# Kernel tuning notes

Hardware: AMD Instinct MI355X
Metric: run time of the kernel (lower is better)

The kernel has to match this reference:

```python
import jax, jax.numpy as jnp
import numpy as np

# ---- static config (mirrors init_kwargs) ----
N, E, G = 10000, 120000, 32
F_NODE, F_EDGE = 64, 16
H, HEADS, L, R = 128, 4, 3, 4
ID_DIM, REL_DIM = 32, 8
NUM_IDS, NUM_CLASSES = 5000, 10
FFN_H, HEAD_H = 256, 128
GRID_SIZE, SPLINE_ORDER = 5, 3
NC = GRID_SIZE + SPLINE_ORDER  # n spline coeffs per input = 8
GRID = jnp.asarray(np.arange(-SPLINE_ORDER, GRID_SIZE + SPLINE_ORDER + 1, dtype=np.float32) * (2.0 / GRID_SIZE) - 1.0)  # [12], grid_range=(-1,1)
NEG = -1e30


def _b_splines(x, grid):
    # x: [B, in] -> bases [B, in, NC]  (Cox-de Boor, as in efficient-kan)
    x = x[..., None]
    bases = ((x >= grid[:-1]) & (x < grid[1:])).astype(x.dtype)
    for p in range(1, SPLINE_ORDER + 1):
        left = (x - grid[:-(p + 1)]) / (grid[p:-1] - grid[:-(p + 1)]) * bases[..., :-1]
        right = (grid[p + 1:] - x) / (grid[p + 1:] - grid[1:-p]) * bases[..., 1:]
        bases = left + right
    return bases


def _kan_linear(x, base_w, spline_w, scaler, grid):
    # base path: SiLU(x) @ W_base^T ; spline path: b_splines(x) contracted with scaled spline weights
    base = jax.nn.silu(x) @ base_w.T
    spline = jnp.einsum('big,oig->bo', _b_splines(x, grid), spline_w * scaler[..., None])
    return base + spline


def _ln(x, g, b, eps=1e-5):
    mu = x.mean(-1, keepdims=True)
    var = ((x - mu) ** 2).mean(-1, keepdims=True)
    return (x - mu) * jax.lax.rsqrt(var + eps) * g + b


def _forward(x, edge_attr, id_emb, in_W, in_b, Wl, bl, Wr, br, We, att, gat_bias,
             rel_gate, rel_emb, ln1_g, ln1_b, ln2_g, ln2_b,
             ffn1_base, ffn1_spline, ffn1_scaler, ffn2_base, ffn2_spline, ffn2_scaler,
             ro_g, ro_b, head1_base, head1_spline, head1_scaler, head2_base, head2_spline, head2_scaler,
             id_token, edge_index, edge_type, batch):
    grid = GRID
    # input proj: concat(id embedding) -> Linear -> SiLU (dropout = identity, eval)
    h = jnp.concatenate([x, id_emb[id_token]], axis=-1)
    h = jax.nn.silu(h @ in_W + in_b)
    src, tgt = edge_index[0], edge_index[1]
    for l in range(L):
        gates = jax.nn.softmax(rel_gate[l])  # all relations present
        h_msg = jnp.zeros_like(h)
        for r in range(R):
            # GATv2Conv (heads=4, concat=False, add_self_loops=False)
            xl = (h @ Wl[l, r] + bl[l, r]).reshape(N, HEADS, H)
            xr = (h @ Wr[l, r] + br[l, r]).reshape(N, HEADS, H)
            # edge feature = concat(edge_attr, rel_emb[r]) @ We, split to avoid materializing the concat
            e = (edge_attr @ We[l, r, :F_EDGE] + rel_emb[l, r] @ We[l, r, F_EDGE:]).reshape(E, HEADS, H)
            z = jax.nn.leaky_relu(xl[src] + xr[tgt] + e, 0.2)   # [E, heads, H]
            score = jnp.einsum('ehd,hd->eh', z, att[l, r])
            mask = (edge_type == r)[:, None]
            score = jnp.where(mask, score, NEG)
            m = jax.ops.segment_max(score, tgt, num_segments=N)  # per-target softmax max
            ex = jnp.where(mask, jnp.exp(score - m[tgt]), 0.0)
            denom = jax.ops.segment_sum(ex, tgt, num_segments=N)
            alpha = ex / jnp.maximum(denom[tgt], 1e-16)          # [E, heads]
            agg = jax.ops.segment_sum(xl[src] * alpha[..., None], tgt, num_segments=N)
            h_r = agg.mean(axis=1) + gat_bias[l, r]              # concat=False -> head mean + bias
            h_msg = h_msg + gates[r] * h_r
        h = _ln(h + h_msg, ln1_g[l], ln1_b[l])
        # KAN FFN: KANLinear(H->FFN_H) -> KANLinear(FFN_H->H)
        h_ffn = _kan_linear(h, ffn1_base[l], ffn1_spline[l], ffn1_scaler[l], grid)
        h_ffn = _kan_linear(h_ffn, ffn2_base[l], ffn2_spline[l], ffn2_scaler[l], grid)
        h = _ln(h + h_ffn, ln2_g[l], ln2_b[l])
    # readout: mean+max pool per graph
    cnt = jax.ops.segment_sum(jnp.ones((N,), h.dtype), batch, num_segments=G)
    h_mean = jax.ops.segment_sum(h, batch, num_segments=G) / jnp.maximum(cnt, 1.0)[:, None]
    h_max = jax.ops.segment_max(h, batch, num_segments=G)
    h_max = jnp.where(jnp.isfinite(h_max), h_max, 0.0)
    g = _ln(jnp.concatenate([h_mean, h_max], axis=-1), ro_g, ro_b)
    # KAN head: KANLinear(2H->HEAD_H) -> KANLinear(HEAD_H->NUM_CLASSES)
    g = _kan_linear(g, head1_base, head1_spline, head1_scaler, grid)
    logits = _kan_linear(g, head2_base, head2_spline, head2_scaler, grid)
    return logits


def setup_inputs():
    key = jax.random.key(0)
    ks = iter(jax.random.split(key, 48))
    n = lambda shape, s=0.05: jax.random.normal(next(ks), shape, dtype=jnp.float32) * s
    d = {}
    d['x'] = jax.random.normal(next(ks), (N, F_NODE), dtype=jnp.float32)
    d['edge_attr'] = jax.random.normal(next(ks), (E, F_EDGE), dtype=jnp.float32)
    d['id_token'] = jax.random.randint(next(ks), (N,), 0, NUM_IDS + 1)
    d['edge_index'] = jax.random.randint(next(ks), (2, E), 0, N)
    d['edge_type'] = jax.random.randint(next(ks), (E,), 0, R)
    d['batch'] = jnp.sort(jax.random.randint(next(ks), (N,), 0, G))
    d['id_emb'] = n((NUM_IDS + 1, ID_DIM), 0.1)
    d['in_W'] = n((F_NODE + ID_DIM, H))
    d['in_b'] = jnp.zeros((H,), jnp.float32)
    d['Wl'] = n((L, R, H, HEADS * H)); d['bl'] = jnp.zeros((L, R, HEADS * H), jnp.float32)
    d['Wr'] = n((L, R, H, HEADS * H)); d['br'] = jnp.zeros((L, R, HEADS * H), jnp.float32)
    d['We'] = n((L, R, F_EDGE + REL_DIM, HEADS * H))
    d['att'] = n((L, R, HEADS, H), 0.1)
    d['gat_bias'] = jnp.zeros((L, R, H), jnp.float32)
    d['rel_gate'] = n((L, R), 0.1)
    d['rel_emb'] = n((L, R, REL_DIM), 0.1)
    d['ln1_g'] = jnp.ones((L, H), jnp.float32); d['ln1_b'] = jnp.zeros((L, H), jnp.float32)
    d['ln2_g'] = jnp.ones((L, H), jnp.float32); d['ln2_b'] = jnp.zeros((L, H), jnp.float32)
    d['ffn1_base'] = n((L, FFN_H, H)); d['ffn1_spline'] = n((L, FFN_H, H, NC)); d['ffn1_scaler'] = jnp.ones((L, FFN_H, H), jnp.float32)
    d['ffn2_base'] = n((L, H, FFN_H)); d['ffn2_spline'] = n((L, H, FFN_H, NC)); d['ffn2_scaler'] = jnp.ones((L, H, FFN_H), jnp.float32)
    d['ro_g'] = jnp.ones((2 * H,), jnp.float32); d['ro_b'] = jnp.zeros((2 * H,), jnp.float32)
    d['head1_base'] = n((HEAD_H, 2 * H)); d['head1_spline'] = n((HEAD_H, 2 * H, NC)); d['head1_scaler'] = jnp.ones((HEAD_H, 2 * H), jnp.float32)
    d['head2_base'] = n((NUM_CLASSES, HEAD_H)); d['head2_spline'] = n((NUM_CLASSES, HEAD_H, NC)); d['head2_scaler'] = jnp.ones((NUM_CLASSES, HEAD_H), jnp.float32)
    return d


def reference(x, edge_attr, id_emb, in_W, in_b, Wl, bl, Wr, br, We, att, gat_bias,
              rel_gate, rel_emb, ln1_g, ln1_b, ln2_g, ln2_b,
              ffn1_base, ffn1_spline, ffn1_scaler, ffn2_base, ffn2_spline, ffn2_scaler,
              ro_g, ro_b, head1_base, head1_spline, head1_scaler, head2_base, head2_spline, head2_scaler,
              id_token, edge_index, edge_type, batch):
    return _forward(x, edge_attr, id_emb, in_W, in_b, Wl, bl, Wr, br, We, att, gat_bias,
                    rel_gate, rel_emb, ln1_g, ln1_b, ln2_g, ln2_b,
                    ffn1_base, ffn1_spline, ffn1_scaler, ffn2_base, ffn2_spline, ffn2_scaler,
                    ro_g, ro_b, head1_base, head1_spline, head1_scaler, head2_base, head2_spline, head2_scaler,
                    id_token, edge_index, edge_type, batch)
```

## Files before the change

### kernel.cpp

```cpp
#include <hip/hip_runtime.h>
#include <cstdint>
#include <cstddef>

#define NN      10000
#define NE      120000
#define NG      32
#define FNODE   64
#define FEDGE   16
#define HID     128
#define NHEADS  4
#define NL      3
#define NR      4
#define IDDIM   32
#define RELDIM  8
#define FFNH    256
#define HEADH   128
#define NCLS    10

#define NCHUNK  128
#define SCTOT   (NN * NR)
#define SCBLK   ((SCTOT + 255) / 256)

typedef __attribute__((ext_vector_type(8))) short short8;
typedef __attribute__((ext_vector_type(4))) float floatx4;

__device__ __forceinline__ float silu_f(float x) { return x / (1.f + expf(-x)); }
__device__ __forceinline__ ushort f2bf(float f) {
  unsigned u = __float_as_uint(f);
  return (ushort)((u + 0x7FFFu + ((u >> 16) & 1u)) >> 16);
}
__device__ __forceinline__ float bf2f(ushort h) { return __uint_as_float((unsigned)h << 16); }

__device__ __forceinline__ void kan_bases(float x, float* out8) {
  float bb[11];
#pragma unroll
  for (int j = 0; j < 11; ++j) {
    float t0 = (j - 3) * 0.4f - 1.f;
    float t1 = (j - 2) * 0.4f - 1.f;
    bb[j] = (x >= t0 && x < t1) ? 1.f : 0.f;
  }
  {
    const float inv = 1.f / 0.4f;
#pragma unroll
    for (int j = 0; j < 10; ++j) {
      float tj = (j - 3) * 0.4f - 1.f, tjp1 = (j - 1) * 0.4f - 1.f;
      bb[j] = ((x - tj) * bb[j] + (tjp1 - x) * bb[j + 1]) * inv;
    }
  }
  {
    const float inv = 1.f / 0.8f;
#pragma unroll
    for (int j = 0; j < 9; ++j) {
      float tj = (j - 3) * 0.4f - 1.f, tjp1 = (j) * 0.4f - 1.f;
      bb[j] = ((x - tj) * bb[j] + (tjp1 - x) * bb[j + 1]) * inv;
    }
  }
  {
    const float inv = 1.f / 1.2000001f;
#pragma unroll
    for (int j = 0; j < 8; ++j) {
      float tj = (j - 3) * 0.4f - 1.f, tjp1 = (j + 1) * 0.4f - 1.f;
      bb[j] = ((x - tj) * bb[j] + (tjp1 - x) * bb[j + 1]) * inv;
    }
  }
#pragma unroll
  for (int j = 0; j < 8; ++j) out8[j] = bb[j];
}

__global__ __launch_bounds__(256) void gemm_bf3(
    const ushort* __restrict__ Ahg, const ushort* __restrict__ Alg,
    const ushort* __restrict__ Bhg, const ushort* __restrict__ Blg,
    const float* __restrict__ bias, float* __restrict__ C,
    int M, int K, int N) {
  constexpr int LDA = 68;
  __shared__ __align__(16) ushort Ah[128 * LDA];
  __shared__ __align__(16) ushort Al[128 * LDA];
  __shared__ __align__(16) ushort Bh[64 * LDA];
  __shared__ __align__(16) ushort Bl[64 * LDA];
  const int tid = threadIdx.x;
  const int lane = tid & 63, wave = tid >> 6;
  const int lrow = lane & 15, quad = lane >> 4;
  const int bm = blockIdx.y * 128, bn = blockIdx.x * 64;
  floatx4 acc[2][4] = {};
  for (int k0 = 0; k0 < K; k0 += 64) {
#pragma unroll
    for (int i = 0; i < 4; ++i) {
      int c = tid + i * 256;
      int row = c >> 3, col8 = c & 7;
      int gr = bm + row;
      uint4 vh = make_uint4(0, 0, 0, 0), vl = make_uint4(0, 0, 0, 0);
      if (gr < M) {
        vh = *(const uint4*)(Ahg + (size_t)gr * K + k0 + col8 * 8);
        vl = *(const uint4*)(Alg + (size_t)gr * K + k0 + col8 * 8);
      }
      *(uint4*)&Ah[row * LDA + col8 * 8] = vh;
      *(uint4*)&Al[row * LDA + col8 * 8] = vl;
    }
#pragma unroll
    for (int i = 0; i < 2; ++i) {
      int c = tid + i * 256;
      int row = c >> 3, col8 = c & 7;
      *(uint4*)&Bh[row * LDA + col8 * 8] = *(const uint4*)(Bhg + (size_t)(bn + row) * K + k0 + col8 * 8);
      *(uint4*)&Bl[row * LDA + col8 * 8] = *(const uint4*)(Blg + (size_t)(bn + row) * K + k0 + col8 * 8);
    }
    __syncthreads();
#pragma unroll
    for (int kk = 0; kk < 64; kk += 32) {
      int kof = kk + quad * 8;
      const int ra0 = (wave * 32 + lrow) * LDA + kof;
      const int ra1 = (wave * 32 + 16 + lrow) * LDA + kof;
      short8 ah0 = *(const short8*)&Ah[ra0];
      short8 ah1 = *(const short8*)&Ah[ra1];
      short8 al0 = *(const short8*)&Al[ra0];
      short8 al1 = *(const short8*)&Al[ra1];
      short8 bh[4], blo[4];
#pragma unroll
      for (int nt = 0; nt < 4; ++nt) {
        int rb = (nt * 16 + lrow) * LDA + kof;
        bh[nt]  = *(const short8*)&Bh[rb];
        blo[nt] = *(const short8*)&Bl[rb];
      }
#pragma unroll
      for (int nt = 0; nt < 4; ++nt) {
        acc[0][nt] = __builtin_amdgcn_mfma_f32_16x16x32_bf16(ah0, bh[nt],  acc[0][nt], 0, 0, 0);
        acc[1][nt] = __builtin_amdgcn_mfma_f32_16x16x32_bf16(ah1, bh[nt],  acc[1][nt], 0, 0, 0);
        acc[0][nt] = __builtin_amdgcn_mfma_f32_16x16x32_bf16(al0, bh[nt],  acc[0][nt], 0, 0, 0);
        acc[1][nt] = __builtin_amdgcn_mfma_f32_16x16x32_bf16(al1, bh[nt],  acc[1][nt], 0, 0, 0);
        acc[0][nt] = __builtin_amdgcn_mfma_f32_16x16x32_bf16(ah0, blo[nt], acc[0][nt], 0, 0, 0);
        acc[1][nt] = __builtin_amdgcn_mfma_f32_16x16x32_bf16(ah1, blo[nt], acc[1][nt], 0, 0, 0);
      }
    }
    __syncthreads();
  }
#pragma unroll
  for (int mt = 0; mt < 2; ++mt) {
#pragma unroll
    for (int nt = 0; nt < 4; ++nt) {
#pragma unroll
      for (int reg = 0; reg < 4; ++reg) {
        int row = bm + wave * 32 + mt * 16 + quad * 4 + reg;
        int col = bn + nt * 16 + lrow;
        if (row < M) {
          float v = acc[mt][nt][reg];
          if (bias) v += bias[col];
          C[(size_t)row * N + col] = v;
        }
      }
    }
  }
}

template<int BM, int SPLIT>
__global__ __launch_bounds__(256) void gemm_kan(
    const float* __restrict__ A, const ushort* __restrict__ Bhg, const ushort* __restrict__ Blg,
    float* __restrict__ C, int M, int In, int N) {
  const int K = In * 9;
  const int ntiles = K >> 6;
  const int per = (ntiles + SPLIT - 1) / SPLIT;
  const int kt0 = blockIdx.z * per;
  const int kt1 = (kt0 + per < ntiles) ? (kt0 + per) : ntiles;
  constexpr int LDA = 68;
  __shared__ __align__(16) ushort Ah[BM * LDA];
  __shared__ __align__(16) ushort Al[BM * LDA];
  __shared__ __align__(16) ushort Bh[64 * LDA];
  __shared__ __align__(16) ushort Bl[64 * LDA];
  const int tid = threadIdx.x;
  const int lane = tid & 63, wave = tid >> 6;
  const int lrow = lane & 15, quad = lane >> 4;
  const int bm = blockIdx.y * BM, bn = blockIdx.x * 64;
  constexpr int MT = BM / 64;
  floatx4 acc[MT][4] = {};
  for (int kt = kt0; kt < kt1; ++kt) {
    int k0 = kt << 6;
    if (k0 < In) {
#pragma unroll
      for (int i = 0; i < BM / 16; ++i) {
        int c = tid + i * 256;
        int row = c >> 4, col4 = c & 15;
        int gr = bm + row;
        float4 v = make_float4(0.f, 0.f, 0.f, 0.f);
        if (gr < M) v = *(const float4*)(A + (size_t)gr * In + k0 + col4 * 4);
        float vv[4] = {silu_f(v.x), silu_f(v.y), silu_f(v.z), silu_f(v.w)};
        ushort h0 = f2bf(vv[0]), h1 = f2bf(vv[1]), h2 = f2bf(vv[2]), h3 = f2bf(vv[3]);
        ushort l0 = f2bf(vv[0] - bf2f(h0)), l1 = f2bf(vv[1] - bf2f(h1));
        ushort l2 = f2bf(vv[2] - bf2f(h2)), l3 = f2bf(vv[3] - bf2f(h3));
        *(uint2*)&Ah[row * LDA + col4 * 4] =
          make_uint2((unsigned)h0 | ((unsigned)h1 << 16), (unsigned)h2 | ((unsigned)h3 << 16));
        *(uint2*)&Al[row * LDA + col4 * 4] =
          make_uint2((unsigned)l0 | ((unsigned)l1 << 16), (unsigned)l2 | ((unsigned)l3 << 16));
      }
    } else {
      int i0 = (k0 - In) >> 3;
      if (tid < BM * 2) {
        int row = tid >> 1, half = tid & 1;
        int gr = bm + row;
        float4 v = make_float4(0.f, 0.f, 0.f, 0.f);
        if (gr < M) v = *(const float4*)(A + (size_t)gr * In + i0 + half * 4);
        float vv[4] = {v.x, v.y, v.z, v.w};
#pragma unroll
        for (int jj = 0; jj < 4; ++jj) {
          float b8[8];
          kan_bases(vv[jj], b8);
          unsigned hu[4], lu[4];
#pragma unroll
          for (int q = 0; q < 4; ++q) {
            ushort ha = f2bf(b8[2 * q]), hb = f2bf(b8[2 * q + 1]);
            ushort la = f2bf(b8[2 * q] - bf2f(ha)), lb = f2bf(b8[2 * q + 1] - bf2f(hb));
            hu[q] = (unsigned)ha | ((unsigned)hb << 16);
            lu[q] = (unsigned)la | ((unsigned)lb << 16);
          }
          int cbase = (half * 4 + jj) * 8;
          *(uint4*)&Ah[row * LDA + cbase] = make_uint4(hu[0], hu[1], hu[2], hu[3]);
          *(uint4*)&Al[row * LDA + cbase] = make_uint4(lu[0], lu[1], lu[2], lu[3]);
        }
      }
    }
#pragma unroll
    for (int i = 0; i < 2; ++i) {
      int c = tid + i * 256;
      int row = c >> 3, col8 = c & 7;
      *(uint4*)&Bh[row * LDA + col8 * 8] = *(const uint4*)(Bhg + (size_t)(bn + row) * K + k0 + col8 * 8);
      *(uint4*)&Bl[row * LDA + col8 * 8] = *(const uint4*)(Blg + (size_t)(bn + row) * K + k0 + col8 * 8);
    }
    __syncthreads();
#pragma unroll
    for (int kk = 0; kk < 64; kk += 32) {
      int kof = kk + quad * 8;
      short8 ah[MT], al[MT];
#pragma unroll
      for (int mt = 0; mt < MT; ++mt) {
        int ra = (wave * (BM / 4) + mt * 16 + lrow) * LDA + kof;
        ah[mt] = *(const short8*)&Ah[ra];
        al[mt] = *(const short8*)&Al[ra];
      }
      short8 bh[4], blo[4];
#pragma unroll
      for (int nt = 0; nt < 4; ++nt) {
        int rb = (nt * 16 + lrow) * LDA + kof;
        bh[nt]  = *(const short8*)&Bh[rb];
        blo[nt] = *(const short8*)&Bl[rb];
      }
#pragma unroll
      for (int nt = 0; nt < 4; ++nt) {
#pragma unroll
        for (int mt = 0; mt < MT; ++mt) {
          acc[mt][nt] = __builtin_amdgcn_mfma_f32_16x16x32_bf16(ah[mt], bh[nt],  acc[mt][nt], 0, 0, 0);
          acc[mt][nt] = __builtin_amdgcn_mfma_f32_16x16x32_bf16(al[mt], bh[nt],  acc[mt][nt], 0, 0, 0);
          acc[mt][nt] = __builtin_amdgcn_mfma_f32_16x16x32_bf16(ah[mt], blo[nt], acc[mt][nt], 0, 0, 0);
        }
      }
    }
    __syncthreads();
  }
#pragma unroll
  for (int mt = 0; mt < MT; ++mt) {
#pragma unroll
    for (int nt = 0; nt < 4; ++nt) {
#pragma unroll
      for (int reg = 0; reg < 4; ++reg) {
        int row = bm + wave * (BM / 4) + mt * 16 + quad * 4 + reg;
        int col = bn + nt * 16 + lrow;
        if (row < M) atomicAdd(&C[(size_t)row * N + col], acc[mt][nt][reg]);
      }
    }
  }
}

__global__ void conv_wT2(const float* __restrict__ Wl, const float* __restrict__ Wr,
                         const float* __restrict__ bl, const float* __restrict__ br,
                         ushort* __restrict__ WTh, ushort* __restrict__ WTl,
                         float* __restrict__ bout, int total) {
  int i = blockIdx.x * 256 + threadIdx.x;
  if (i >= total) return;
  int g2 = i / (2048 * 128), rem = i % (2048 * 128);
  int n = rem >> 7, k = rem & 127;
  int l = g2 >> 1, pair = g2 & 1;
  int r = pair * 2 + (n >> 10);
  int nsub = n & 1023;
  int nn = nsub & 511;
  int g = l * NR + r;
  const float* W = (nsub < 512) ? Wl : Wr;
  float v = W[(size_t)g * 65536 + (size_t)k * 512 + nn];
  ushort hi = f2bf(v);
  WTh[i] = hi;
  WTl[i] = f2bf(v - bf2f(hi));
  if (k == 0) bout[g2 * 2048 + n] = ((nsub < 512) ? bl : br)[g * 512 + nn];
}

__global__ void build_kan_wT(const float* __restrict__ base_w, const float* __restrict__ spline_w,
                             const float* __restrict__ scaler,
                             ushort* __restrict__ BTh, ushort* __restrict__ BTl,
                             int In, int Out) {
  int i = blockIdx.x * 256 + threadIdx.x;
  if (i >= In * 9 * Out) return;
  int o = i / (In * 9), k = i % (In * 9);
  float v;
  if (k < In) v = base_w[(size_t)o * In + k];
  else {
    int q = k - In, ii = q >> 3, gq = q & 7;
    v = spline_w[((size_t)o * In + ii) * 8 + gq] * scaler[(size_t)o * In + ii];
  }
  ushort hi = f2bf(v);
  BTh[i] = hi;
  BTl[i] = f2bf(v - bf2f(hi));
}

__global__ __launch_bounds__(128) void input_proj(
    const float* __restrict__ x, const float* __restrict__ id_emb,
    const int* __restrict__ id_token, const float* __restrict__ inW,
    const float* __restrict__ inb, float* __restrict__ h,
    ushort* __restrict__ hh, ushort* __restrict__ hl) {
  int n = blockIdx.x, j = threadIdx.x;
  __shared__ float s[FNODE + IDDIM];
  if (j < FNODE) s[j] = x[(size_t)n * FNODE + j];
  else if (j < FNODE + IDDIM) s[j] = id_emb[(size_t)id_token[n] * IDDIM + (j - FNODE)];
  __syncthreads();
  float acc = inb[j];
#pragma unroll
  for (int k = 0; k < FNODE + IDDIM; ++k) acc = fmaf(s[k], inW[k * HID + j], acc);
  float v = silu_f(acc);
  h[(size_t)n * HID + j] = v;
  ushort hi = f2bf(v);
  hh[(size_t)n * HID + j] = hi;
  hl[(size_t)n * HID + j] = f2bf(v - bf2f(hi));
}

__global__ __launch_bounds__(512) void layer_prep(
    const float* __restrict__ rel_gate, const float* __restrict__ gat_bias,
    const float* __restrict__ rel_emb, const float* __restrict__ We, int l,
    float* __restrict__ gates, float* __restrict__ msg_bias, float* __restrict__ erel) {
  int j = threadIdx.x;
  float g[NR]; float mx = -1e30f;
  for (int r = 0; r < NR; ++r) { g[r] = rel_gate[l * NR + r]; mx = fmaxf(mx, g[r]); }
  float s = 0.f;
  for (int r = 0; r < NR; ++r) { g[r] = expf(g[r] - mx); s += g[r]; }
  for (int r = 0; r < NR; ++r) g[r] /= s;
  if (j < NR) gates[j] = g[j];
  if (j < HID) {
    float b = 0.f;
    for (int r = 0; r < NR; ++r) b = fmaf(g[r], gat_bias[((size_t)(l * NR + r)) * HID + j], b);
    msg_bias[j] = b;
  }
  for (int r = 0; r < NR; ++r) {
    const float* Wer = We + ((size_t)(l * NR + r)) * 24 * 512;
    const float* re  = rel_emb + (l * NR + r) * RELDIM;
    float acc = 0.f;
#pragma unroll
    for (int q = 0; q < RELDIM; ++q) acc = fmaf(re[q], Wer[(FEDGE + q) * 512 + j], acc);
    erel[r * 512 + j] = acc;
  }
}

__global__ void fill_zero(float* __restrict__ p, int n) {
  int i = blockIdx.x * 256 + threadIdx.x;
  if (i < n) p[i] = 0.f;
}
__global__ void fill_zero_i(int* __restrict__ p, int n) {
  int i = blockIdx.x * 256 + threadIdx.x;
  if (i < n) p[i] = 0;
}

__global__ void csr_count2(const int* __restrict__ eidx, const int* __restrict__ etype,
                           int* __restrict__ deg2) {
  int e = blockIdx.x * 256 + threadIdx.x;
  if (e < NE) atomicAdd(&deg2[eidx[NE + e] * NR + etype[e]], 1);
}

__global__ __launch_bounds__(256) void scan_p1(const int* __restrict__ deg2,
                                               int* __restrict__ tmp_incl, int* __restrict__ bsum) {
  __shared__ int ps[256];
  int t = threadIdx.x, blk = blockIdx.x;
  int i = blk * 256 + t;
  int v = (i < SCTOT) ? deg2[i] : 0;
  ps[t] = v;
  __syncthreads();
  for (int o = 1; o < 256; o <<= 1) {
    int u = (t >= o) ? ps[t - o] : 0;
    __syncthreads();
    ps[t] += u;
    __syncthreads();
  }
  if (i < SCTOT) tmp_incl[i] = ps[t];
  if (t == 255) bsum[blk] = ps[255];
}
__global__ __launch_bounds__(256) void scan_p2(const int* __restrict__ bsum, int* __restrict__ boff) {
  __shared__ int ps[256];
  int t = threadIdx.x;
  int v = (t < SCBLK) ? bsum[t] : 0;
  ps[t] = v;
  __syncthreads();
  for (int o = 1; o < 256; o <<= 1) {
    int u = (t >= o) ? ps[t - o] : 0;
    __syncthreads();
    ps[t] += u;
    __syncthreads();
  }
  if (t < SCBLK) boff[t] = ps[t] - v;
}
__global__ __launch_bounds__(256) void scan_p3(const int* __restrict__ deg2,
                                               const int* __restrict__ tmp_incl,
                                               const int* __restrict__ boff,
                                               int* __restrict__ in_off2, int* __restrict__ cursor2) {
  int t = threadIdx.x, blk = blockIdx.x;
  int i = blk * 256 + t;
  if (i < SCTOT) {
    int excl = boff[blk] + tmp_incl[i] - deg2[i];
    in_off2[i] = excl;
    cursor2[i] = excl;
  }
  if (i == 0) in_off2[SCTOT] = NE;
}

__global__ void csr_scatter2(const int* __restrict__ eidx, const int* __restrict__ etype,
                             int* __restrict__ cursor2,
                             int* __restrict__ in_e2, int* __restrict__ in_s2) {
  int e = blockIdx.x * 256 + threadIdx.x;
  if (e < NE) {
    int pos = atomicAdd(&cursor2[eidx[NE + e] * NR + etype[e]], 1);
    in_e2[pos] = e;
    in_s2[pos] = eidx[e];
  }
}

__global__ __launch_bounds__(256) void gat_node4(
    const int* __restrict__ in_off2, const int* __restrict__ in_e2, const int* __restrict__ in_s2,
    const float* __restrict__ eattr, const float* __restrict__ xlr,
    const float* __restrict__ We_base, const float* __restrict__ erel_base,
    const float* __restrict__ att_base, const float* __restrict__ gates,
    int rbase, float* __restrict__ hmsg) {
  __shared__ float WeL[16][512];
  __shared__ float attL[512];
  __shared__ float erelL[512];
  int tid = threadIdx.x;
  int rs = blockIdx.y;
  int r = rbase + rs;
  const float* We_r = We_base + (size_t)rs * 24 * 512;
  for (int i = tid; i < 16 * 512; i += 256) WeL[i >> 9][i & 511] = We_r[i];
  for (int i = tid; i < 512; i += 256) {
    attL[i] = att_base[rs * 512 + i];
    erelL[i] = erel_base[rs * 512 + i];
  }
  __syncthreads();
  float gr = gates[r] * 0.25f;
  int lane = tid & 63, wave = tid >> 6;
  int n = blockIdx.x * 4 + wave;
  if (n >= NN) return;
  int roff = rs * 1024;
  float xr[8];
  const float* xrb = xlr + (size_t)n * 2048 + roff + 512;
#pragma unroll
  for (int h = 0; h < 4; ++h) {
    xr[h * 2]     = xrb[h * 128 + lane];
    xr[h * 2 + 1] = xrb[h * 128 + 64 + lane];
  }
  float m[4] = {-1e30f, -1e30f, -1e30f, -1e30f};
  float lsum[4] = {0.f, 0.f, 0.f, 0.f};
  float acc[8] = {0.f, 0.f, 0.f, 0.f, 0.f, 0.f, 0.f, 0.f};
  int e0 = in_off2[n * NR + r], e1 = in_off2[n * NR + r + 1];
  int e_nxt = 0, s_nxt = 0;
  if (e0 < e1) { e_nxt = in_e2[e0]; s_nxt = in_s2[e0]; }
  for (int ii = e0; ii < e1; ++ii) {
    int e = e_nxt, s = s_nxt;
    if (ii + 1 < e1) { e_nxt = in_e2[ii + 1]; s_nxt = in_s2[ii + 1]; }
    const float* xls = xlr + (size_t)s * 2048 + roff;
    float ea[16];
#pragma unroll
    for (int k = 0; k < 16; ++k) ea[k] = eattr[(size_t)e * 16 + k];
    float xlv[8], p[4];
#pragma unroll
    for (int h = 0; h < 4; ++h) {
      float ph = 0.f;
#pragma unroll
      for (int half = 0; half < 2; ++half) {
        int idx = h * 128 + half * 64 + lane;
        float xv = xls[idx];
        xlv[h * 2 + half] = xv;
        float et = erelL[idx];
#pragma unroll
        for (int k = 0; k < 16; ++k) et = fmaf(ea[k], WeL[k][idx], et);
        float z = xv + xr[h * 2 + half] + et;
        z = (z > 0.f) ? z : 0.2f * z;
        ph = fmaf(z, attL[idx], ph);
      }
      p[h] = ph;
    }
#pragma unroll
    for (int h = 0; h < 4; ++h) {
#pragma unroll
      for (int o = 32; o > 0; o >>= 1) p[h] += __shfl_xor(p[h], o, 64);
    }
#pragma unroll
    for (int h = 0; h < 4; ++h) {
      float sh = p[h];
      float mn = fmaxf(m[h], sh);
      float sc = expf(m[h] - mn);
      float we = expf(sh - mn);
      m[h] = mn;
      lsum[h] = lsum[h] * sc + we;
      acc[h * 2]     = acc[h * 2] * sc + we * xlv[h * 2];
      acc[h * 2 + 1] = acc[h * 2 + 1] * sc + we * xlv[h * 2 + 1];
    }
  }
  float o0 = 0.f, o1 = 0.f;
#pragma unroll
  for (int h = 0; h < 4; ++h) {
    float inv = 1.f / fmaxf(lsum[h], 1e-16f);
    o0 += acc[h * 2] * inv;
    o1 += acc[h * 2 + 1] * inv;
  }
  size_t base = (size_t)n * HID;
  atomicAdd(&hmsg[base + lane],      gr * o0);
  atomicAdd(&hmsg[base + 64 + lane], gr * o1);
}

__global__ __launch_bounds__(64) void ln128(
    float* __restrict__ h, const float* __restrict__ add, const float* __restrict__ bvec,
    const float* __restrict__ g, const float* __restrict__ b,
    ushort* __restrict__ hh, ushort* __restrict__ hl) {
  int n = blockIdx.x, lane = threadIdx.x;
  size_t base = (size_t)n * HID;
  float x0 = h[base + lane] + add[base + lane];
  float x1 = h[base + 64 + lane] + add[base + 64 + lane];
  if (bvec) { x0 += bvec[lane]; x1 += bvec[64 + lane]; }
  float s = x0 + x1;
#pragma unroll
  for (int m = 32; m > 0; m >>= 1) s += __shfl_xor(s, m, 64);
  float mu = s * (1.f / 128.f);
  float d0 = x0 - mu, d1 = x1 - mu;
  float q = d0 * d0 + d1 * d1;
#pragma unroll
  for (int m = 32; m > 0; m >>= 1) q += __shfl_xor(q, m, 64);
  float inv = 1.f / sqrtf(q * (1.f / 128.f) + 1e-5f);
  float o0 = d0 * inv * g[lane] + b[lane];
  float o1 = d1 * inv * g[64 + lane] + b[64 + lane];
  h[base + lane]      = o0;
  h[base + 64 + lane] = o1;
  if (hh) {
    ushort i0 = f2bf(o0), i1 = f2bf(o1);
    hh[base + lane] = i0;        hh[base + 64 + lane] = i1;
    hl[base + lane] = f2bf(o0 - bf2f(i0));
    hl[base + 64 + lane] = f2bf(o1 - bf2f(i1));
  }
}

__global__ void expand_f32(const float* __restrict__ v, float* __restrict__ u, int In, int rows) {
  int i = blockIdx.x * 256 + threadIdx.x;
  if (i >= rows * In) return;
  int n = i / In, c = i % In;
  float x = v[(size_t)n * In + c];
  size_t base = (size_t)n * In * 9;
  u[base + c] = silu_f(x);
  float b8[8];
  kan_bases(x, b8);
  float* ub = u + base + In + (size_t)c * 8;
#pragma unroll
  for (int gq = 0; gq < 8; ++gq) ub[gq] = b8[gq];
}

__global__ __launch_bounds__(128) void pool_part(
    const float* __restrict__ h, const int* __restrict__ batch,
    float* __restrict__ psum, float* __restrict__ pmax, float* __restrict__ pcnt) {
  __shared__ float sS[NG][HID];
  __shared__ float sM[NG][HID];
  __shared__ int sC[NG];
  int d = threadIdx.x, blk = blockIdx.x;
  const float NEGINF = __uint_as_float(0xff800000u);
  for (int i = d; i < NG * HID; i += 128) {
    ((float*)sS)[i] = 0.f;
    ((float*)sM)[i] = NEGINF;
  }
  if (d < NG) sC[d] = 0;
  __syncthreads();
  const int CH = (NN + NCHUNK - 1) / NCHUNK;
  int n0 = blk * CH, n1 = (n0 + CH < NN) ? n0 + CH : NN;
  for (int n = n0; n < n1; ++n) {
    int g = batch[n];
    float v = h[(size_t)n * HID + d];
    sS[g][d] += v;
    sM[g][d] = fmaxf(sM[g][d], v);
    if (d == 0) sC[g]++;
  }
  __syncthreads();
  for (int i = d; i < NG * HID; i += 128) {
    psum[(size_t)blk * NG * HID + i] = ((float*)sS)[i];
    pmax[(size_t)blk * NG * HID + i] = ((float*)sM)[i];
  }
  if (d < NG) pcnt[blk * NG + d] = (float)sC[d];
}

__global__ __launch_bounds__(256) void pool_final2(
    const float* __restrict__ psum, const float* __restrict__ pmax,
    const float* __restrict__ pcnt, const float* __restrict__ rog,
    const float* __restrict__ rob, float* __restrict__ gvec) {
  int g = blockIdx.x, j = threadIdx.x;
  __shared__ float rb[256];
  float x;
  if (j < HID) {
    float s = 0.f, cn = 0.f;
    for (int c = 0; c < NCHUNK; ++c) {
      s += psum[(size_t)c * NG * HID + g * HID + j];
      cn += pcnt[c * NG + g];
    }
    x = s / fmaxf(cn, 1.f);
  } else {
    float mx = __uint_as_float(0xff800000u);
    for (int c = 0; c < NCHUNK; ++c)
      mx = fmaxf(mx, pmax[(size_t)c * NG * HID + g * HID + (j - HID)]);
    x = (mx > -1e38f) ? mx : 0.f;
  }
  rb[j] = x; __syncthreads();
  for (int st = 128; st > 0; st >>= 1) { if (j < st) rb[j] += rb[j + st]; __syncthreads(); }
  float mu = rb[0] * (1.f / 256.f); __syncthreads();
  float d = x - mu;
  rb[j] = d * d; __syncthreads();
  for (int st = 128; st > 0; st >>= 1) { if (j < st) rb[j] += rb[j + st]; __syncthreads(); }
  float var = rb[0] * (1.f / 256.f);
  float inv = 1.f / sqrtf(var + 1e-5f);
  gvec[(size_t)g * 256 + j] = d * inv * rog[j] + rob[j];
}

__global__ __launch_bounds__(256) void kan_head_w(
    const float* __restrict__ u, const float* __restrict__ base_w,
    const float* __restrict__ spline_w, const float* __restrict__ scaler,
    float* __restrict__ out, int In, int Out, int npairs) {
  int wid = blockIdx.x * 4 + (threadIdx.x >> 6);
  if (wid >= npairs) return;
  int g = wid / Out, o = wid % Out;
  int lane = threadIdx.x & 63;
  const float* ug = u + (size_t)g * In * 9;
  const float* bw = base_w + (size_t)o * In;
  const float* sp = spline_w + (size_t)o * In * 8;
  const float* sc = scaler + (size_t)o * In;
  float acc = 0.f;
  for (int i = lane; i < In; i += 64) acc = fmaf(ug[i], bw[i], acc);
  const float* us = ug + In;
  for (int k = lane; k < In * 8; k += 64) {
    int i = k >> 3;
    acc = fmaf(us[k], sp[k] * sc[i], acc);
  }
#pragma unroll
  for (int off2 = 32; off2 > 0; off2 >>= 1) acc += __shfl_xor(acc, off2, 64);
  if (lane == 0) out[(size_t)g * Out + o] = acc;
}

extern "C" void kernel_launch(void* const* d_in, const int* in_sizes, int n_in,
                              void* d_out, int out_size, void* d_ws, size_t ws_size,
                              hipStream_t stream) {
  const float* x         = (const float*)d_in[0];
  const float* edge_attr = (const float*)d_in[1];
  const int*   id_token  = (const int*)  d_in[2];
  const int*   edge_index= (const int*)  d_in[3];
  const int*   edge_type = (const int*)  d_in[4];
  const int*   batch     = (const int*)  d_in[5];
  const float* id_emb    = (const float*)d_in[6];
  const float* inW       = (const float*)d_in[7];
  const float* inb       = (const float*)d_in[8];
  const float* Wl        = (const float*)d_in[9];
  const float* bl        = (const float*)d_in[10];
  const float* Wr        = (const float*)d_in[11];
  const float* br        = (const float*)d_in[12];
  const float* We        = (const float*)d_in[13];
  const float* att       = (const float*)d_in[14];
  const float* gat_bias  = (const float*)d_in[15];
  const float* rel_gate  = (const float*)d_in[16];
  const float* rel_emb   = (const float*)d_in[17];
  const float* ln1g      = (const float*)d_in[18];
  const float* ln1b      = (const float*)d_in[19];
  const float* ln2g      = (const float*)d_in[20];
  const float* ln2b      = (const float*)d_in[21];
  const float* ffn1_base = (const float*)d_in[22];
  const float* ffn1_spl  = (const float*)d_in[23];
  const float* ffn1_sc   = (const float*)d_in[24];
  const float* ffn2_base = (const float*)d_in[25];
  const float* ffn2_spl  = (const float*)d_in[26];
  const float* ffn2_sc   = (const float*)d_in[27];
  const float* rog       = (const float*)d_in[28];
  const float* rob       = (const float*)d_in[29];
  const float* h1_base   = (const float*)d_in[30];
  const float* h1_spl    = (const float*)d_in[31];
  const float* h1_sc     = (const float*)d_in[32];
  const float* h2_base   = (const float*)d_in[33];
  const float* h2_spl    = (const float*)d_in[34];
  const float* h2_sc     = (const float*)d_in[35];
  (void)in_sizes; (void)n_in; (void)out_size; (void)ws_size;

  char* wsp = (char*)d_ws;
  size_t off = 0;
  auto carve = [&](size_t bytes) { char* p = wsp + off; off = (off + bytes + 255) & ~(size_t)255; return p; };
  float*    h     = (float*)   carve((size_t)NN * HID * 4);
  ushort*   h_hi  = (ushort*)  carve((size_t)NN * HID * 2);
  ushort*   h_lo  = (ushort*)  carve((size_t)NN * HID * 2);
  float*    hmsg  = (float*)   carve((size_t)NN * HID * 4);
  float*    t1    = (float*)   carve((size_t)NN * FFNH * 4);
  float*    gates = (float*)   carve(NR * 4);
  float*    msgb  = (float*)   carve(HID * 4);
  float*    erel  = (float*)   carve(NR * 512 * 4);
  ushort*   WTh   = (ushort*)  carve((size_t)NL * 2 * 2048 * HID * 2);
  ushort*   WTl   = (ushort*)  carve((size_t)NL * 2 * 2048 * HID * 2);
  float*    blr   = (float*)   carve((size_t)NL * 2 * 2048 * 4);
  ushort*   B1h   = (ushort*)  carve((size_t)FFNH * HID * 9 * 2);
  ushort*   B1l   = (ushort*)  carve((size_t)FFNH * HID * 9 * 2);
  ushort*   B2h   = (ushort*)  carve((size_t)HID * FFNH * 9 * 2);
  ushort*   B2l   = (ushort*)  carve((size_t)HID * FFNH * 9 * 2);
  float*    psum  = (float*)   carve((size_t)NCHUNK * NG * HID * 4);
  float*    pmax  = (float*)   carve((size_t)NCHUNK * NG * HID * 4);
  float*    pcnt  = (float*)   carve((size_t)NCHUNK * NG * 4);
  float*    gvec  = (float*)   carve((size_t)NG * 256 * 4);
  float*    uhead = (float*)   carve((size_t)NG * 256 * 9 * 4);
  float*    thead = (float*)   carve((size_t)NG * HEADH * 4);
  float*    xlr   = (float*)   carve((size_t)NN * 2048 * 4);
  int*      deg2  = (int*)     carve((size_t)SCTOT * 4);
  int*      in_off2=(int*)     carve((size_t)(SCTOT + 1) * 4);
  int*      cursor2=(int*)     carve((size_t)SCTOT * 4);
  int*      tmp_incl=(int*)    carve((size_t)SCTOT * 4);
  int*      bsum  = (int*)     carve((size_t)SCBLK * 4);
  int*      boff  = (int*)     carve((size_t)SCBLK * 4);
  int*      in_e2 = (int*)     carve((size_t)NE * 4);
  int*      in_s2 = (int*)     carve((size_t)NE * 4);

  fill_zero_i<<<(SCTOT + 255) / 256, 256, 0, stream>>>(deg2, SCTOT);
  csr_count2<<<(NE + 255) / 256, 256, 0, stream>>>(edge_index, edge_type, deg2);
  scan_p1<<<SCBLK, 256, 0, stream>>>(deg2, tmp_incl, bsum);
  scan_p2<<<1, 256, 0, stream>>>(bsum, boff);
  scan_p3<<<SCBLK, 256, 0, stream>>>(deg2, tmp_incl, boff, in_off2, cursor2);
  csr_scatter2<<<(NE + 255) / 256, 256, 0, stream>>>(edge_index, edge_type, cursor2, in_e2, in_s2);

  {
    int total = NL * 2 * 2048 * 128;
    conv_wT2<<<(total + 255) / 256, 256, 0, stream>>>(Wl, Wr, bl, br, WTh, WTl, blr, total);
  }

  input_proj<<<NN, 128, 0, stream>>>(x, id_emb, id_token, inW, inb, h, h_hi, h_lo);

  const int MB128 = (NN + 127) / 128;
  const int MB64  = (NN + 63) / 64;
  for (int l = 0; l < NL; ++l) {
    layer_prep<<<1, 512, 0, stream>>>(rel_gate, gat_bias, rel_emb, We, l, gates, msgb, erel);
    fill_zero<<<(NN * HID + 255) / 256, 256, 0, stream>>>(hmsg, NN * HID);
    for (int pair = 0; pair < 2; ++pair) {
      int g2 = l * 2 + pair;
      const ushort* WThp = WTh + (size_t)g2 * 2048 * HID;
      const ushort* WTlp = WTl + (size_t)g2 * 2048 * HID;
      const float* blp   = blr + (size_t)g2 * 2048;
      int rbase = pair * 2;
      gemm_bf3<<<dim3(2048 / 64, MB128), 256, 0, stream>>>(h_hi, h_lo, WThp, WTlp, blp, xlr, NN, HID, 2048);
      gat_node4<<<dim3((NN + 3) / 4, 2), 256, 0, stream>>>(
          in_off2, in_e2, in_s2, edge_attr, xlr,
          We + ((size_t)(l * NR + rbase)) * 24 * 512, erel + rbase * 512,
          att + (size_t)(l * NR + rbase) * 512, gates, rbase, hmsg);
    }
    ln128<<<NN, 64, 0, stream>>>(h, hmsg, msgb, ln1g + l * HID, ln1b + l * HID, nullptr, nullptr);

    build_kan_wT<<<((HID * 9 * FFNH) + 255) / 256, 256, 0, stream>>>(
        ffn1_base + (size_t)l * FFNH * HID, ffn1_spl + (size_t)l * FFNH * HID * 8,
        ffn1_sc + (size_t)l * FFNH * HID, B1h, B1l, HID, FFNH);
    fill_zero<<<(NN * FFNH + 255) / 256, 256, 0, stream>>>(t1, NN * FFNH);
    gemm_kan<128, 3><<<dim3(FFNH / 64, MB128, 3), 256, 0, stream>>>(h, B1h, B1l, t1, NN, HID, FFNH);
    build_kan_wT<<<((FFNH * 9 * HID) + 255) / 256, 256, 0, stream>>>(
        ffn2_base + (size_t)l * HID * FFNH, ffn2_spl + (size_t)l * HID * FFNH * 8,
        ffn2_sc + (size_t)l * HID * FFNH, B2h, B2l, FFNH, HID);
    fill_zero<<<(NN * HID + 255) / 256, 256, 0, stream>>>(hmsg, NN * HID);
    gemm_kan<64, 4><<<dim3(HID / 64, MB64, 4), 256, 0, stream>>>(t1, B2h, B2l, hmsg, NN, FFNH, HID);
    ln128<<<NN, 64, 0, stream>>>(h, hmsg, nullptr, ln2g + l * HID, ln2b + l * HID, h_hi, h_lo);
  }

  pool_part<<<NCHUNK, 128, 0, stream>>>(h, batch, psum, pmax, pcnt);
  pool_final2<<<NG, 256, 0, stream>>>(psum, pmax, pcnt, rog, rob, gvec);
  expand_f32<<<((NG * 256) + 255) / 256, 256, 0, stream>>>(gvec, uhead, 256, NG);
  {
    int npairs = NG * HEADH;
    kan_head_w<<<(npairs + 3) / 4, 256, 0, stream>>>(uhead, h1_base, h1_spl, h1_sc, thead, 256, HEADH, npairs);
  }
  expand_f32<<<((NG * HEADH) + 255) / 256, 256, 0, stream>>>(thead, uhead, HEADH, NG);
  {
    int npairs = NG * NCLS;
    kan_head_w<<<(npairs + 3) / 4, 256, 0, stream>>>(uhead, h2_base, h2_spl, h2_sc, (float*)d_out, HEADH, NCLS, npairs);
  }
}
```

Measured before the change: 1.626 ms.

## Vectorize GAT edge kernel with float4 per-lane channel layout and prefetch

```diff
diff --git a/kernel.cpp b/kernel.cpp
--- a/kernel.cpp
+++ b/kernel.cpp
@@ -422,92 +422,115 @@
   }
 }
 
-__global__ __launch_bounds__(256) void gat_node4(
+__global__ __launch_bounds__(256) void gat_node6(
     const int* __restrict__ in_off2, const int* __restrict__ in_e2, const int* __restrict__ in_s2,
     const float* __restrict__ eattr, const float* __restrict__ xlr,
     const float* __restrict__ We_base, const float* __restrict__ erel_base,
     const float* __restrict__ att_base, const float* __restrict__ gates,
     int rbase, float* __restrict__ hmsg) {
-  __shared__ float WeL[16][512];
-  __shared__ float attL[512];
-  __shared__ float erelL[512];
+  __shared__ __align__(16) float WeL[16 * 512];
+  __shared__ __align__(16) float sAgg[4][512];
   int tid = threadIdx.x;
   int rs = blockIdx.y;
   int r = rbase + rs;
   const float* We_r = We_base + (size_t)rs * 24 * 512;
-  for (int i = tid; i < 16 * 512; i += 256) WeL[i >> 9][i & 511] = We_r[i];
-  for (int i = tid; i < 512; i += 256) {
-    attL[i] = att_base[rs * 512 + i];
-    erelL[i] = erel_base[rs * 512 + i];
-  }
+  for (int i = tid; i < 16 * 512 / 4; i += 256)
+    *(float4*)&WeL[i * 4] = *(const float4*)&We_r[i * 4];
   __syncthreads();
   float gr = gates[r] * 0.25f;
   int lane = tid & 63, wave = tid >> 6;
   int n = blockIdx.x * 4 + wave;
   if (n >= NN) return;
   int roff = rs * 1024;
-  float xr[8];
+  const int cA = lane * 4;
+  const int cB = 256 + lane * 4;
   const float* xrb = xlr + (size_t)n * 2048 + roff + 512;
-#pragma unroll
-  for (int h = 0; h < 4; ++h) {
-    xr[h * 2]     = xrb[h * 128 + lane];
-    xr[h * 2 + 1] = xrb[h * 128 + 64 + lane];
-  }
-  float m[4] = {-1e30f, -1e30f, -1e30f, -1e30f};
-  float lsum[4] = {0.f, 0.f, 0.f, 0.f};
-  float acc[8] = {0.f, 0.f, 0.f, 0.f, 0.f, 0.f, 0.f, 0.f};
-  int e0 = in_off2[n * NR + r], e1 = in_off2[n * NR + r + 1];
-  int e_nxt = 0, s_nxt = 0;
-  if (e0 < e1) { e_nxt = in_e2[e0]; s_nxt = in_s2[e0]; }
-  for (int ii = e0; ii < e1; ++ii) {
-    int e = e_nxt, s = s_nxt;
-    if (ii + 1 < e1) { e_nxt = in_e2[ii + 1]; s_nxt = in_s2[ii + 1]; }
-    const float* xls = xlr + (size_t)s * 2048 + roff;
-    float ea[16];
-#pragma unroll
-    for (int k = 0; k < 16; ++k) ea[k] = eattr[(size_t)e * 16 + k];
-    float xlv[8], p[4];
-#pragma unroll
-    for (int h = 0; h < 4; ++h) {
-      float ph = 0.f;
-#pragma unroll
-      for (int half = 0; half < 2; ++half) {
-        int idx = h * 128 + half * 64 + lane;
-        float xv = xls[idx];
-        xlv[h * 2 + half] = xv;
-        float et = erelL[idx];
-#pragma unroll
-        for (int k = 0; k < 16; ++k) et = fmaf(ea[k], WeL[k][idx], et);
-        float z = xv + xr[h * 2 + half] + et;
-        z = (z > 0.f) ? z : 0.2f * z;
-        ph = fmaf(z, attL[idx], ph);
-      }
-      p[h] = ph;
-    }
-#pragma unroll
-    for (int h = 0; h < 4; ++h) {
-#pragma unroll
-      for (int o = 32; o > 0; o >>= 1) p[h] += __shfl_xor(p[h], o, 64);
-    }
-#pragma unroll
-    for (int h = 0; h < 4; ++h) {
-      float sh = p[h];
-      float mn = fmaxf(m[h], sh);
-      float sc = expf(m[h] - mn);
-      float we = expf(sh - mn);
-      m[h] = mn;
-      lsum[h] = lsum[h] * sc + we;
-      acc[h * 2]     = acc[h * 2] * sc + we * xlv[h * 2];
-      acc[h * 2 + 1] = acc[h * 2 + 1] * sc + we * xlv[h * 2 + 1];
-    }
-  }
-  float o0 = 0.f, o1 = 0.f;
-#pragma unroll
-  for (int h = 0; h < 4; ++h) {
-    float inv = 1.f / fmaxf(lsum[h], 1e-16f);
-    o0 += acc[h * 2] * inv;
-    o1 += acc[h * 2 + 1] * inv;
-  }
+  float4 xrA = *(const float4*)(xrb + cA);
+  float4 xrB = *(const float4*)(xrb + cB);
+  float4 attA = *(const float4*)(att_base + rs * 512 + cA);
+  float4 attB = *(const float4*)(att_base + rs * 512 + cB);
+  float4 erA  = *(const float4*)(erel_base + rs * 512 + cA);
+  float4 erB  = *(const float4*)(erel_base + rs * 512 + cB);
+  float mA = -1e30f, mB = -1e30f, lsA = 0.f, lsB = 0.f;
+  float4 accA = make_float4(0.f, 0.f, 0.f, 0.f);
+  float4 accB = make_float4(0.f, 0.f, 0.f, 0.f);
+  int e0 = in_off2[n * NR + r];
+  int cnt = in_off2[n * NR + r + 1] - e0;
+  float4 pxA, pxB, pe0, pe1, pe2, pe3;
+  int eN = 0, sN = 0;
+  if (cnt > 0) {
+    int eC = in_e2[e0], sC = in_s2[e0];
+    if (cnt > 1) { eN = in_e2[e0 + 1]; sN = in_s2[e0 + 1]; }
+    const float* xls = xlr + (size_t)sC * 2048 + roff;
+    pxA = *(const float4*)(xls + cA);
+    pxB = *(const float4*)(xls + cB);
+    const float4* eap = (const float4*)(eattr + (size_t)eC * 16);
+    pe0 = eap[0]; pe1 = eap[1]; pe2 = eap[2]; pe3 = eap[3];
+  }
+  for (int j = 0; j < cnt; ++j) {
+    float4 xA = pxA, xB = pxB;
+    float ea[16] = {pe0.x, pe0.y, pe0.z, pe0.w, pe1.x, pe1.y, pe1.z, pe1.w,
+                    pe2.x, pe2.y, pe2.z, pe2.w, pe3.x, pe3.y, pe3.z, pe3.w};
+    if (j + 1 < cnt) {
+      int eC = eN, sC = sN;
+      if (j + 2 < cnt) { eN = in_e2[e0 + j + 2]; sN = in_s2[e0 + j + 2]; }
+      const float* xls = xlr + (size_t)sC * 2048 + roff;
+      pxA = *(const float4*)(xls + cA);
+      pxB = *(const float4*)(xls + cB);
+      const float4* eap = (const float4*)(eattr + (size_t)eC * 16);
+      pe0 = eap[0]; pe1 = eap[1]; pe2 = eap[2]; pe3 = eap[3];
+    }
+    float4 etA = erA, etB = erB;
+#pragma unroll
+    for (int k = 0; k < 16; ++k) {
+      float4 wA = *(const float4*)&WeL[k * 512 + cA];
+      float4 wB = *(const float4*)&WeL[k * 512 + cB];
+      etA.x = fmaf(ea[k], wA.x, etA.x); etA.y = fmaf(ea[k], wA.y, etA.y);
+      etA.z = fmaf(ea[k], wA.z, etA.z); etA.w = fmaf(ea[k], wA.w, etA.w);
+      etB.x = fmaf(ea[k], wB.x, etB.x); etB.y = fmaf(ea[k], wB.y, etB.y);
+      etB.z = fmaf(ea[k], wB.z, etB.z); etB.w = fmaf(ea[k], wB.w, etB.w);
+    }
+    float sA, sB;
+    {
+      float z0 = xA.x + xrA.x + etA.x; z0 = (z0 > 0.f) ? z0 : 0.2f * z0;
+      float z1 = xA.y + xrA.y + etA.y; z1 = (z1 > 0.f) ? z1 : 0.2f * z1;
+      float z2 = xA.z + xrA.z + etA.z; z2 = (z2 > 0.f) ? z2 : 0.2f * z2;
+      float z3 = xA.w + xrA.w + etA.w; z3 = (z3 > 0.f) ? z3 : 0.2f * z3;
+      sA = z0 * attA.x + z1 * attA.y + z2 * attA.z + z3 * attA.w;
+      z0 = xB.x + xrB.x + etB.x; z0 = (z0 > 0.f) ? z0 : 0.2f * z0;
+      z1 = xB.y + xrB.y + etB.y; z1 = (z1 > 0.f) ? z1 : 0.2f * z1;
+      z2 = xB.z + xrB.z + etB.z; z2 = (z2 > 0.f) ? z2 : 0.2f * z2;
+      z3 = xB.w + xrB.w + etB.w; z3 = (z3 > 0.f) ? z3 : 0.2f * z3;
+      sB = z0 * attB.x + z1 * attB.y + z2 * attB.z + z3 * attB.w;
+    }
+#pragma unroll
+    for (int o = 1; o <= 16; o <<= 1) {
+      sA += __shfl_xor(sA, o, 64);
+      sB += __shfl_xor(sB, o, 64);
+    }
+    {
+      float mn = fmaxf(mA, sA);
+      float sc = expf(mA - mn), we = expf(sA - mn);
+      mA = mn; lsA = lsA * sc + we;
+      accA.x = accA.x * sc + we * xA.x; accA.y = accA.y * sc + we * xA.y;
+      accA.z = accA.z * sc + we * xA.z; accA.w = accA.w * sc + we * xA.w;
+    }
+    {
+      float mn = fmaxf(mB, sB);
+      float sc = expf(mB - mn), we = expf(sB - mn);
+      mB = mn; lsB = lsB * sc + we;
+      accB.x = accB.x * sc + we * xB.x; accB.y = accB.y * sc + we * xB.y;
+      accB.z = accB.z * sc + we * xB.z; accB.w = accB.w * sc + we * xB.w;
+    }
+  }
+  float invA = 1.f / fmaxf(lsA, 1e-16f);
+  float invB = 1.f / fmaxf(lsB, 1e-16f);
+  *(float4*)&sAgg[wave][cA] = make_float4(accA.x * invA, accA.y * invA, accA.z * invA, accA.w * invA);
+  *(float4*)&sAgg[wave][cB] = make_float4(accB.x * invB, accB.y * invB, accB.z * invB, accB.w * invB);
+  float o0 = sAgg[wave][lane]       + sAgg[wave][128 + lane]
+           + sAgg[wave][256 + lane] + sAgg[wave][384 + lane];
+  float o1 = sAgg[wave][64 + lane]  + sAgg[wave][192 + lane]
+           + sAgg[wave][320 + lane] + sAgg[wave][448 + lane];
   size_t base = (size_t)n * HID;
   atomicAdd(&hmsg[base + lane],      gr * o0);
   atomicAdd(&hmsg[base + 64 + lane], gr * o1);
@@ -744,7 +767,7 @@
       const float* blp   = blr + (size_t)g2 * 2048;
       int rbase = pair * 2;
       gemm_bf3<<<dim3(2048 / 64, MB128), 256, 0, stream>>>(h_hi, h_lo, WThp, WTlp, blp, xlr, NN, HID, 2048);
-      gat_node4<<<dim3((NN + 3) / 4, 2), 256, 0, stream>>>(
+      gat_node6<<<dim3((NN + 3) / 4, 2), 256, 0, stream>>>(
           in_off2, in_e2, in_s2, edge_attr, xlr,
           We + ((size_t)(l * NR + rbase)) * 24 * 512, erel + rbase * 512,
           att + (size_t)(l * NR + rbase) * 512, gates, rbase, hmsg);
```

Result: faster. 1.492 ms (-8.3%).
